# Optimization experiments

Hardware: AMD Instinct MI355X
Metric: run time of the kernel (lower is better)

The kernel has to match this reference:

```python
import jax, jax.numpy as jnp
import numpy as np

B, C, L = 8, 256, 2048        # batch, query_dim, seq len
HEADS, DIM_HEAD = 4, 32
HIDDEN = HEADS * DIM_HEAD      # 128
EPS = 1e-05
SCALE = DIM_HEAD ** -0.5


def setup_inputs() -> dict:
    key = jax.random.key(0)
    ks = jax.random.split(key, 8)
    s_in = 1.0 / np.sqrt(C)
    s_h = 1.0 / np.sqrt(HIDDEN)
    return {
        "x": jax.random.normal(ks[0], (B, C, L), dtype=jnp.float32),
        "g": jnp.ones((1, C, 1), dtype=jnp.float32),
        "b": jnp.zeros((1, C, 1), dtype=jnp.float32),
        "Wq": jax.random.normal(ks[1], (HIDDEN, C), dtype=jnp.float32) * s_in,
        "Wk": jax.random.normal(ks[2], (HIDDEN, C), dtype=jnp.float32) * s_in,
        "Wv": jax.random.normal(ks[3], (HIDDEN, C), dtype=jnp.float32) * s_in,
        "Wo": jax.random.normal(ks[4], (C, HIDDEN), dtype=jnp.float32) * s_h,
        "bo": jnp.zeros((C,), dtype=jnp.float32),
    }


def reference(x, g, b, Wq, Wk, Wv, Wo, bo):
    og_x = x
    # channel-dim LayerNorm (dim=1), biased variance
    mean = jnp.mean(x, axis=1, keepdims=True)
    var = jnp.var(x, axis=1, keepdims=True)
    xn = (x - mean) / jnp.sqrt(var + EPS) * g + b          # [B, C, L]
    xt = jnp.transpose(xn, (0, 2, 1))                      # [B, L, C]
    # QKV projections (self-attention: context = normed x)
    q = xt @ Wq.T                                          # [B, L, HIDDEN]
    k = xt @ Wk.T
    v = xt @ Wv.T
    # b (h c) d layout: [B, HEADS, DIM_HEAD, L]
    split = lambda t: jnp.transpose(t, (0, 2, 1)).reshape(B, HEADS, DIM_HEAD, L)
    q, k, v = split(q), split(k), split(v)
    # scores over head-channel dim c -> [B, H, L, L]
    qk = jnp.einsum('bhcd,bhce->bhde', q, k) * SCALE
    attn = jax.nn.softmax(qk, axis=-1)
    out = jnp.einsum('bhde,bhce->bhcd', attn, v)           # [B, H, DIM_HEAD, L]
    out = out.reshape(B, HIDDEN, L)
    # 1x1 Conv1d: hidden -> query_dim
    y = jnp.einsum('oc,bcl->bol', Wo, out) + bo[None, :, None]
    return y + og_x
```

## Files before the change

kernel.cpp:

```cpp
#include <hip/hip_runtime.h>
#include <math.h>

#define BB_ 8
#define CC_ 256
#define LL_ 2048
#define HEADS_ 4
#define DHEAD_ 32
#define HID_ 128
#define EPS_ 1e-5f
#define SCALE_ 0.17677669529663687f
#define K1_ (SCALE_ * 1.44269504088896f)

typedef short v8s  __attribute__((ext_vector_type(8)));
typedef float v4f  __attribute__((ext_vector_type(4)));
typedef float v16f __attribute__((ext_vector_type(16)));
typedef unsigned v4u __attribute__((ext_vector_type(4)));

__device__ inline short f2bf(float x) {
    union { float f; unsigned u; } a; a.f = x;
    unsigned r = a.u + 0x7fffu + ((a.u >> 16) & 1u);
    return (short)(r >> 16);
}
__device__ inline unsigned fbits(float x) { union { float f; unsigned u; } a; a.f = x; return a.u; }

__global__ __launch_bounds__(256) void k_prep(
    const float* __restrict__ Wq, const float* __restrict__ Wk, const float* __restrict__ Wv,
    const float* __restrict__ Wo, const float* __restrict__ g, const float* __restrict__ bvec,
    short* __restrict__ wqkv, short* __restrict__ wo, float2* __restrict__ gb)
{
    __shared__ float red0[256], red1[256];
    const int blk = blockIdx.x, c = threadIdx.x;
    if (blk < 384) {
        const float* W; int oo; float scale = 1.f;
        if (blk < 128)      { W = Wq; oo = blk;       scale = K1_; }
        else if (blk < 256) { W = Wk; oo = blk - 128; }
        else                { W = Wv; oo = blk - 256; }
        float w  = W[oo * 256 + c] * scale;
        float wg = w * g[c];
        wqkv[blk * 256 + c] = f2bf(wg);
        red0[c] = wg;
        red1[c] = w * bvec[c];
        __syncthreads();
        for (int s = 128; s > 0; s >>= 1) {
            if (c < s) { red0[c] += red0[c + s]; red1[c] += red1[c + s]; }
            __syncthreads();
        }
        if (c == 0) gb[blk] = make_float2(red0[0], red1[0]);
    } else {
        int i2 = (blk - 384) * 256 + c;
        wo[i2] = f2bf(Wo[i2]);
    }
}

__global__ __launch_bounds__(512) void k_ln_qkv(
    const float* __restrict__ x, const short* __restrict__ wqkv, const float2* __restrict__ gb,
    short* __restrict__ q, short* __restrict__ k, short* __restrict__ v)
{
    __shared__ float xn[CC_ * 33];
    __shared__ short xnT[32 * 264];
    __shared__ short st2[128 * 48];
    __shared__ float ps_[8 * 32], ps2_[8 * 32];
    __shared__ float rs_s[32], rsmu_s[32];
    const int b   = blockIdx.y;
    const int l0  = blockIdx.x * 32;
    const int tid = threadIdx.x;
    const int wave = tid >> 6, lane = tid & 63;

    {
        const int ls = tid & 31;
        float s = 0.f, s2 = 0.f;
        #pragma unroll
        for (int kk = 0; kk < 16; ++kk) {
            int c = (tid >> 5) + 16 * kk;
            float t = x[((size_t)b * CC_ + c) * LL_ + l0 + ls];
            xn[c * 33 + ls] = t;
            s += t; s2 += t * t;
        }
        s  += __shfl_xor(s, 32, 64);
        s2 += __shfl_xor(s2, 32, 64);
        if (lane < 32) { ps_[wave * 32 + lane] = s; ps2_[wave * 32 + lane] = s2; }
    }
    __syncthreads();
    if (tid < 32) {
        float s = 0.f, s2 = 0.f;
        #pragma unroll
        for (int p = 0; p < 8; ++p) { s += ps_[p * 32 + tid]; s2 += ps2_[p * 32 + tid]; }
        float mean = s * (1.f / CC_);
        float var  = s2 * (1.f / CC_) - mean * mean;
        float rs   = rsqrtf(var + EPS_);
        rs_s[tid]   = rs;
        rsmu_s[tid] = rs * mean;
    }
    for (int idx = tid; idx < 32 * 128; idx += 512) {
        int ls = idx >> 7, cc = idx & 127;
        int c0 = 2 * cc;
        xnT[ls * 264 + c0]     = f2bf(xn[c0 * 33 + ls]);
        xnT[ls * 264 + c0 + 1] = f2bf(xn[(c0 + 1) * 33 + ls]);
    }
    __syncthreads();

    const int n = lane & 15, quad = lane >> 4;
    const int rowbase = (wave >> 2) * 16;
    const int colbase = (wave & 3) * 96;

    v4f acc[6];
    #pragma unroll
    for (int ct = 0; ct < 6; ++ct) acc[ct] = (v4f){0.f, 0.f, 0.f, 0.f};

    #pragma unroll
    for (int ks = 0; ks < 8; ++ks) {
        const v8s af = *(const v8s*)(xnT + (rowbase + n) * 264 + ks * 32 + quad * 8);
        #pragma unroll
        for (int ct = 0; ct < 6; ++ct) {
            const v8s bfrag = *(const v8s*)(wqkv + (size_t)(colbase + ct * 16 + n) * 256 + ks * 32 + quad * 8);
            acc[ct] = __builtin_amdgcn_mfma_f32_16x16x32_bf16(af, bfrag, acc[ct], 0, 0, 0);
        }
    }
    __syncthreads();

    float rsv[4], rmv[4];
    #pragma unroll
    for (int r = 0; r < 4; ++r) {
        int l = rowbase + quad * 4 + r;
        rsv[r] = rs_s[l]; rmv[r] = rsmu_s[l];
    }
    #pragma unroll
    for (int ct = 0; ct < 6; ++ct) {
        int o = colbase + ct * 16 + n;
        float2 gbo = gb[o];
        #pragma unroll
        for (int r = 0; r < 4; ++r) {
            int l = rowbase + quad * 4 + r;
            float val = rsv[r] * acc[ct][r] - rmv[r] * gbo.x + gbo.y;
            if (o < 256)      xnT[l * 264 + o] = f2bf(val);
            else              st2[(o - 256) * 48 + l] = f2bf(val);
        }
    }
    __syncthreads();

    {
        int u = tid;
        int h = u >> 7, rest = u & 127;
        int l = rest >> 2, dg = rest & 3;
        size_t bh = (size_t)b * HEADS_ + h;
        v8s qv = *(const v8s*)(xnT + l * 264 + h * 32 + dg * 8);
        *(v8s*)(q + (bh * LL_ + l0 + l) * DHEAD_ + dg * 8) = qv;
        v8s kv = *(const v8s*)(xnT + l * 264 + 128 + h * 32 + dg * 8);
        *(v8s*)(k + (bh * LL_ + l0 + l) * DHEAD_ + dg * 8) = kv;

        int op = u >> 2, lg = u & 3;
        v8s vv = *(const v8s*)(st2 + op * 48 + lg * 8);
        int h2 = op >> 5, d = op & 31;
        *(v8s*)(v + (((size_t)b * HEADS_ + h2) * DHEAD_ + d) * LL_ + l0 + lg * 8) = vv;
    }
}

__global__ __launch_bounds__(512) void k_attn(
    const short* __restrict__ q, const short* __restrict__ k, const short* __restrict__ v,
    short* __restrict__ ao)
{
    __shared__ float Ost[4][32][32];
    __shared__ float psumst[4 * 32];
    const int bh   = blockIdx.y;
    const int b    = bh >> 2, h = bh & 3;
    const int tid  = threadIdx.x;
    const int wave = tid >> 6, lane = tid & 63;
    const int wq   = wave & 3;
    const int kh   = wave >> 2;
    const int m    = lane & 31;
    const int half = lane >> 5;
    const size_t kvbase = (size_t)bh * LL_ * DHEAD_;
    const size_t vbase  = (size_t)bh * DHEAD_ * LL_;

    const int q0 = blockIdx.x * 128 + wq * 32;
    const int kb = kh * 1024;

    const v8s qf0 = *(const v8s*)(q + kvbase + (size_t)(q0 + m) * DHEAD_ + half * 8);
    const v8s qf1 = *(const v8s*)(q + kvbase + (size_t)(q0 + m) * DHEAD_ + 16 + half * 8);

    v16f O = {};
    float psum = 0.f;

    #define LDK_(pos, off) (*(const v8s*)(k + kvbase + (size_t)((pos) + m) * DHEAD_ + (off) + half * 8))
    #define LDV_(pos, off) (*(const v8s*)(v + vbase + (size_t)m * LL_ + (pos) + (off) + half * 8))

    v8s vf0 = LDV_(kb, 0), vf1 = LDV_(kb, 16);
    v8s kn0 = LDK_(kb + 32, 0), kn1 = LDK_(kb + 32, 16);
    v16f S;
    {
        v8s kf0 = LDK_(kb, 0), kf1 = LDK_(kb, 16);
        S = __builtin_amdgcn_mfma_f32_32x32x16_bf16(kf0, qf0, (v16f){}, 0, 0, 0);
        S = __builtin_amdgcn_mfma_f32_32x32x16_bf16(kf1, qf1, S,        0, 0, 0);
    }

    for (int kt = 0; kt < 1024; kt += 32) {
        const int ktn = kb + ((kt + 32) & 1023);
        const int kt2 = kb + ((kt + 64) & 1023);
        v16f Sn = __builtin_amdgcn_mfma_f32_32x32x16_bf16(kn0, qf0, (v16f){}, 0, 0, 0);
        Sn      = __builtin_amdgcn_mfma_f32_32x32x16_bf16(kn1, qf1, Sn,        0, 0, 0);
        kn0 = LDK_(kt2, 0); kn1 = LDK_(kt2, 16);
        v8s vn0 = LDV_(ktn, 0), vn1 = LDV_(ktn, 16);

        unsigned e[8];
        #pragma unroll
        for (int i = 0; i < 8; ++i) {
            float pa = __builtin_amdgcn_exp2f(S[2 * i]);
            float pb = __builtin_amdgcn_exp2f(S[2 * i + 1]);
            psum += pa + pb;
            e[i] = __builtin_amdgcn_perm(fbits(pb) + 0x8000u, fbits(pa) + 0x8000u, 0x07060302u);
        }
        v4u f1, f2;
#if __has_builtin(__builtin_amdgcn_permlane32_swap)
        {
            auto r02 = __builtin_amdgcn_permlane32_swap(e[0], e[2], false, false);
            auto r13 = __builtin_amdgcn_permlane32_swap(e[1], e[3], false, false);
            auto r46 = __builtin_amdgcn_permlane32_swap(e[4], e[6], false, false);
            auto r57 = __builtin_amdgcn_permlane32_swap(e[5], e[7], false, false);
            f1 = (v4u){r02[0], r13[0], r02[1], r13[1]};
            f2 = (v4u){r46[0], r57[0], r46[1], r57[1]};
        }
#else
        {
            unsigned o0 = __shfl_xor(e[0], 32, 64), o1 = __shfl_xor(e[1], 32, 64);
            unsigned o2 = __shfl_xor(e[2], 32, 64), o3 = __shfl_xor(e[3], 32, 64);
            unsigned o4 = __shfl_xor(e[4], 32, 64), o5 = __shfl_xor(e[5], 32, 64);
            unsigned o6 = __shfl_xor(e[6], 32, 64), o7 = __shfl_xor(e[7], 32, 64);
            f1 = half ? (v4u){o2, o3, e[2], e[3]} : (v4u){e[0], e[1], o0, o1};
            f2 = half ? (v4u){o6, o7, e[6], e[7]} : (v4u){e[4], e[5], o4, o5};
        }
#endif
        O = __builtin_amdgcn_mfma_f32_32x32x16_bf16(__builtin_bit_cast(v8s, f1), vf0, O, 0, 0, 0);
        O = __builtin_amdgcn_mfma_f32_32x32x16_bf16(__builtin_bit_cast(v8s, f2), vf1, O, 0, 0, 0);

        S = Sn; vf0 = vn0; vf1 = vn1;
    }
    #undef LDK_
    #undef LDV_

    psum += __shfl_xor(psum, 32, 64);

    if (kh == 1) {
        #pragma unroll
        for (int r = 0; r < 16; ++r) {
            int qr = (r & 3) + 8 * (r >> 2) + 4 * half;
            Ost[wq][qr][m] = O[r];
        }
        if (half == 0) psumst[wq * 32 + m] = psum;
    }
    __syncthreads();
    if (kh == 0) {
        float den = psum + psumst[wq * 32 + m];
        float invden = 1.f / den;
        #pragma unroll
        for (int r = 0; r < 16; ++r) {
            int qr = (r & 3) + 8 * (r >> 2) + 4 * half;
            float inv = __shfl(invden, qr, 64);
            float val = (O[r] + Ost[wq][qr][m]) * inv;
            int row = q0 + qr;
            ao[((size_t)b * LL_ + row) * HID_ + h * DHEAD_ + m] = f2bf(val);
        }
    }
}

__global__ __launch_bounds__(256) void k_oproj(
    const short* __restrict__ ao, const short* __restrict__ wo, const float* __restrict__ bo,
    const float* __restrict__ x, float* __restrict__ out)
{
    const int b = blockIdx.z;
    const int l0 = blockIdx.x * 16;
    const int obase = blockIdx.y * 8;
    const int tid = threadIdx.x;
    const int wave = tid >> 6, lane = tid & 63;
    const int n = lane & 15, quad = lane >> 4;

    v8s bf[4];
    #pragma unroll
    for (int ks = 0; ks < 4; ++ks)
        bf[ks] = *(const v8s*)(ao + ((size_t)b * LL_ + l0 + n) * HID_ + ks * 32 + quad * 8);

    #pragma unroll
    for (int oi_ = 0; oi_ < 2; ++oi_) {
        int ot = obase + wave * 2 + oi_;
        v4f acc = {0.f, 0.f, 0.f, 0.f};
        #pragma unroll
        for (int ks = 0; ks < 4; ++ks) {
            const v8s af = *(const v8s*)(wo + (size_t)(ot * 16 + n) * HID_ + ks * 32 + quad * 8);
            acc = __builtin_amdgcn_mfma_f32_16x16x32_bf16(af, bf[ks], acc, 0, 0, 0);
        }
        #pragma unroll
        for (int r = 0; r < 4; ++r) {
            int o = ot * 16 + quad * 4 + r;
            size_t oi = ((size_t)b * CC_ + o) * LL_ + l0 + n;
            out[oi] = acc[r] + bo[o] + x[oi];
        }
    }
}

extern "C" void kernel_launch(void* const* d_in, const int* in_sizes, int n_in,
                              void* d_out, int out_size, void* d_ws, size_t ws_size,
                              hipStream_t stream) {
    const float* x  = (const float*)d_in[0];
    const float* g  = (const float*)d_in[1];
    const float* bv = (const float*)d_in[2];
    const float* Wq = (const float*)d_in[3];
    const float* Wk = (const float*)d_in[4];
    const float* Wv = (const float*)d_in[5];
    const float* Wo = (const float*)d_in[6];
    const float* bo = (const float*)d_in[7];
    float* out = (float*)d_out;

    const size_t qkv_elems = (size_t)BB_ * HEADS_ * LL_ * DHEAD_;
    short* q    = (short*)d_ws;
    short* k    = q + qkv_elems;
    short* v    = k + qkv_elems;
    short* ao   = v + qkv_elems;
    short* wqkv = ao + qkv_elems;
    short* wo   = wqkv + 384 * 256;
    float2* gb  = (float2*)(wo + 256 * 128);

    k_prep  <<<dim3(512), dim3(256), 0, stream>>>(Wq, Wk, Wv, Wo, g, bv, wqkv, wo, gb);
    k_ln_qkv<<<dim3(LL_ / 32, BB_), dim3(512), 0, stream>>>(x, wqkv, gb, q, k, v);
    k_attn  <<<dim3(LL_ / 128, BB_ * HEADS_), dim3(512), 0, stream>>>(q, k, v, ao);
    k_oproj <<<dim3(LL_ / 16, 2, BB_), dim3(256), 0, stream>>>(ao, wo, bo, x, out);
}
```

Before: 173.6 us.

## Stage K/V chunks in shared memory and drop split-key reduction in attention

Result: faster. 166.7 us (-4.0%).

```diff
diff --git a/kernel.cpp b/kernel.cpp
--- a/kernel.cpp
+++ b/kernel.cpp
@@ -155,25 +155,23 @@
     }
 }
 
-__global__ __launch_bounds__(512) void k_attn(
+#define CHK_ 256
+__global__ __launch_bounds__(256) void k_attn(
     const short* __restrict__ q, const short* __restrict__ k, const short* __restrict__ v,
     short* __restrict__ ao)
 {
-    __shared__ float Ost[4][32][32];
-    __shared__ float psumst[4 * 32];
+    __shared__ short Kb[CHK_ * 40];
+    __shared__ short Vb[32 * 264];
     const int bh   = blockIdx.y;
     const int b    = bh >> 2, h = bh & 3;
     const int tid  = threadIdx.x;
     const int wave = tid >> 6, lane = tid & 63;
-    const int wq   = wave & 3;
-    const int kh   = wave >> 2;
     const int m    = lane & 31;
     const int half = lane >> 5;
     const size_t kvbase = (size_t)bh * LL_ * DHEAD_;
     const size_t vbase  = (size_t)bh * DHEAD_ * LL_;
 
-    const int q0 = blockIdx.x * 128 + wq * 32;
-    const int kb = kh * 1024;
+    const int q0 = blockIdx.x * 128 + wave * 32;
 
     const v8s qf0 = *(const v8s*)(q + kvbase + (size_t)(q0 + m) * DHEAD_ + half * 8);
     const v8s qf1 = *(const v8s*)(q + kvbase + (size_t)(q0 + m) * DHEAD_ + 16 + half * 8);
@@ -181,84 +179,77 @@
     v16f O = {};
     float psum = 0.f;
 
-    #define LDK_(pos, off) (*(const v8s*)(k + kvbase + (size_t)((pos) + m) * DHEAD_ + (off) + half * 8))
-    #define LDV_(pos, off) (*(const v8s*)(v + vbase + (size_t)m * LL_ + (pos) + (off) + half * 8))
-
-    v8s vf0 = LDV_(kb, 0), vf1 = LDV_(kb, 16);
-    v8s kn0 = LDK_(kb + 32, 0), kn1 = LDK_(kb + 32, 16);
-    v16f S;
-    {
-        v8s kf0 = LDK_(kb, 0), kf1 = LDK_(kb, 16);
-        S = __builtin_amdgcn_mfma_f32_32x32x16_bf16(kf0, qf0, (v16f){}, 0, 0, 0);
-        S = __builtin_amdgcn_mfma_f32_32x32x16_bf16(kf1, qf1, S,        0, 0, 0);
-    }
-
-    for (int kt = 0; kt < 1024; kt += 32) {
-        const int ktn = kb + ((kt + 32) & 1023);
-        const int kt2 = kb + ((kt + 64) & 1023);
-        v16f Sn = __builtin_amdgcn_mfma_f32_32x32x16_bf16(kn0, qf0, (v16f){}, 0, 0, 0);
-        Sn      = __builtin_amdgcn_mfma_f32_32x32x16_bf16(kn1, qf1, Sn,        0, 0, 0);
-        kn0 = LDK_(kt2, 0); kn1 = LDK_(kt2, 16);
-        v8s vn0 = LDV_(ktn, 0), vn1 = LDV_(ktn, 16);
-
-        unsigned e[8];
-        #pragma unroll
-        for (int i = 0; i < 8; ++i) {
-            float pa = __builtin_amdgcn_exp2f(S[2 * i]);
-            float pb = __builtin_amdgcn_exp2f(S[2 * i + 1]);
-            psum += pa + pb;
-            e[i] = __builtin_amdgcn_perm(fbits(pb) + 0x8000u, fbits(pa) + 0x8000u, 0x07060302u);
-        }
-        v4u f1, f2;
+    for (int kc = 0; kc < LL_; kc += CHK_) {
+        __syncthreads();
+        {
+            const short* src = k + kvbase + (size_t)(kc + tid) * DHEAD_;
+            short* dst = Kb + tid * 40;
+            #pragma unroll
+            for (int j = 0; j < 4; ++j)
+                *(v8s*)(dst + j * 8) = *(const v8s*)(src + j * 8);
+        }
+        {
+            const int col = (tid & 31) * 8, dr = tid >> 5;
+            #pragma unroll
+            for (int p = 0; p < 4; ++p) {
+                int d = p * 8 + dr;
+                *(v8s*)(Vb + d * 264 + col) =
+                    *(const v8s*)(v + vbase + (size_t)d * LL_ + kc + col);
+            }
+        }
+        __syncthreads();
+
+        #pragma unroll
+        for (int ktl = 0; ktl < CHK_; ktl += 32) {
+            const v8s kf0 = *(const v8s*)(Kb + (ktl + m) * 40 + half * 8);
+            const v8s kf1 = *(const v8s*)(Kb + (ktl + m) * 40 + 16 + half * 8);
+            v16f S = __builtin_amdgcn_mfma_f32_32x32x16_bf16(kf0, qf0, (v16f){}, 0, 0, 0);
+            S      = __builtin_amdgcn_mfma_f32_32x32x16_bf16(kf1, qf1, S,        0, 0, 0);
+
+            const v8s vf0 = *(const v8s*)(Vb + m * 264 + ktl + half * 8);
+            const v8s vf1 = *(const v8s*)(Vb + m * 264 + ktl + 16 + half * 8);
+
+            unsigned e[8];
+            #pragma unroll
+            for (int i = 0; i < 8; ++i) {
+                float pa = __builtin_amdgcn_exp2f(S[2 * i]);
+                float pb = __builtin_amdgcn_exp2f(S[2 * i + 1]);
+                psum += pa + pb;
+                e[i] = __builtin_amdgcn_perm(fbits(pb) + 0x8000u, fbits(pa) + 0x8000u, 0x07060302u);
+            }
+            v4u f1, f2;
 #if __has_builtin(__builtin_amdgcn_permlane32_swap)
-        {
-            auto r02 = __builtin_amdgcn_permlane32_swap(e[0], e[2], false, false);
-            auto r13 = __builtin_amdgcn_permlane32_swap(e[1], e[3], false, false);
-            auto r46 = __builtin_amdgcn_permlane32_swap(e[4], e[6], false, false);
-            auto r57 = __builtin_amdgcn_permlane32_swap(e[5], e[7], false, false);
-            f1 = (v4u){r02[0], r13[0], r02[1], r13[1]};
-            f2 = (v4u){r46[0], r57[0], r46[1], r57[1]};
-        }
+            {
+                auto r02 = __builtin_amdgcn_permlane32_swap(e[0], e[2], false, false);
+                auto r13 = __builtin_amdgcn_permlane32_swap(e[1], e[3], false, false);
+                auto r46 = __builtin_amdgcn_permlane32_swap(e[4], e[6], false, false);
+                auto r57 = __builtin_amdgcn_permlane32_swap(e[5], e[7], false, false);
+                f1 = (v4u){r02[0], r13[0], r02[1], r13[1]};
+                f2 = (v4u){r46[0], r57[0], r46[1], r57[1]};
+            }
 #else
-        {
-            unsigned o0 = __shfl_xor(e[0], 32, 64), o1 = __shfl_xor(e[1], 32, 64);
-            unsigned o2 = __shfl_xor(e[2], 32, 64), o3 = __shfl_xor(e[3], 32, 64);
-            unsigned o4 = __shfl_xor(e[4], 32, 64), o5 = __shfl_xor(e[5], 32, 64);
-            unsigned o6 = __shfl_xor(e[6], 32, 64), o7 = __shfl_xor(e[7], 32, 64);
-            f1 = half ? (v4u){o2, o3, e[2], e[3]} : (v4u){e[0], e[1], o0, o1};
-            f2 = half ? (v4u){o6, o7, e[6], e[7]} : (v4u){e[4], e[5], o4, o5};
-        }
+            {
+                unsigned o0 = __shfl_xor(e[0], 32, 64), o1 = __shfl_xor(e[1], 32, 64);
+                unsigned o2 = __shfl_xor(e[2], 32, 64), o3 = __shfl_xor(e[3], 32, 64);
+                unsigned o4 = __shfl_xor(e[4], 32, 64), o5 = __shfl_xor(e[5], 32, 64);
+                unsigned o6 = __shfl_xor(e[6], 32, 64), o7 = __shfl_xor(e[7], 32, 64);
+                f1 = half ? (v4u){o2, o3, e[2], e[3]} : (v4u){e[0], e[1], o0, o1};
+                f2 = half ? (v4u){o6, o7, e[6], e[7]} : (v4u){e[4], e[5], o4, o5};
+            }
 #endif
-        O = __builtin_amdgcn_mfma_f32_32x32x16_bf16(__builtin_bit_cast(v8s, f1), vf0, O, 0, 0, 0);
-        O = __builtin_amdgcn_mfma_f32_32x32x16_bf16(__builtin_bit_cast(v8s, f2), vf1, O, 0, 0, 0);
-
-        S = Sn; vf0 = vn0; vf1 = vn1;
-    }
-    #undef LDK_
-    #undef LDV_
+            O = __builtin_amdgcn_mfma_f32_32x32x16_bf16(__builtin_bit_cast(v8s, f1), vf0, O, 0, 0, 0);
+            O = __builtin_amdgcn_mfma_f32_32x32x16_bf16(__builtin_bit_cast(v8s, f2), vf1, O, 0, 0, 0);
+        }
+    }
 
     psum += __shfl_xor(psum, 32, 64);
-
-    if (kh == 1) {
-        #pragma unroll
-        for (int r = 0; r < 16; ++r) {
-            int qr = (r & 3) + 8 * (r >> 2) + 4 * half;
-            Ost[wq][qr][m] = O[r];
-        }
-        if (half == 0) psumst[wq * 32 + m] = psum;
-    }
-    __syncthreads();
-    if (kh == 0) {
-        float den = psum + psumst[wq * 32 + m];
-        float invden = 1.f / den;
-        #pragma unroll
-        for (int r = 0; r < 16; ++r) {
-            int qr = (r & 3) + 8 * (r >> 2) + 4 * half;
-            float inv = __shfl(invden, qr, 64);
-            float val = (O[r] + Ost[wq][qr][m]) * inv;
-            int row = q0 + qr;
-            ao[((size_t)b * LL_ + row) * HID_ + h * DHEAD_ + m] = f2bf(val);
-        }
+    float invden = 1.f / psum;
+    #pragma unroll
+    for (int r = 0; r < 16; ++r) {
+        int qr = (r & 3) + 8 * (r >> 2) + 4 * half;
+        float inv = __shfl(invden, qr, 64);
+        int row = q0 + qr;
+        ao[((size_t)b * LL_ + row) * HID_ + h * DHEAD_ + m] = f2bf(O[r] * inv);
     }
 }
 
@@ -320,6 +311,6 @@
 
     k_prep  <<<dim3(512), dim3(256), 0, stream>>>(Wq, Wk, Wv, Wo, g, bv, wqkv, wo, gb);
     k_ln_qkv<<<dim3(LL_ / 32, BB_), dim3(512), 0, stream>>>(x, wqkv, gb, q, k, v);
-    k_attn  <<<dim3(LL_ / 128, BB_ * HEADS_), dim3(512), 0, stream>>>(q, k, v, ao);
+    k_attn  <<<dim3(LL_ / 128, BB_ * HEADS_), dim3(256), 0, stream>>>(q, k, v, ao);
     k_oproj <<<dim3(LL_ / 16, 2, BB_), dim3(256), 0, stream>>>(ao, wo, bo, x, out);
 }
```
